# Kernel optimization log

Measured on AMD Instinct MI355X. Metric: run time of the kernel, lower is better.

The kernel has to match this reference:

```python
import jax, jax.numpy as jnp
import numpy as np

N_GRID = 128
DX = 1.0 / N_GRID
INV_DX = float(N_GRID)
DT = 1e-4
P_VOL = (DX * 0.5) ** 2
P_RHO = 1.0
P_MASS = P_VOL * P_RHO
E_MOD, NU = 1000.0, 0.2
MU_0 = E_MOD / (2.0 * (1.0 + NU))
LAMBDA_0 = E_MOD * NU / ((1.0 + NU) * (1.0 - 2.0 * NU))
N_PART = 1_000_000


def setup_inputs() -> dict:
    key = jax.random.key(0)
    k1, k2, k3, k4, k5 = jax.random.split(key, 5)
    # particles strictly inside the domain so the 3x3 stencil stays in-grid
    x = 0.1 + 0.8 * jax.random.uniform(k1, (N_PART, 2), jnp.float32)
    v = 0.5 * jax.random.normal(k2, (N_PART, 2), jnp.float32)
    C = 0.1 * jax.random.normal(k3, (N_PART, 2, 2), jnp.float32)
    F = jnp.eye(2, dtype=jnp.float32)[None] + 0.01 * jax.random.normal(k4, (N_PART, 2, 2), jnp.float32)
    material = jax.random.randint(k5, (N_PART,), 0, 3, jnp.int32)
    Jp = jnp.ones((N_PART,), jnp.float32)
    return {"x": x, "v": v, "C": C, "F": F, "material": material, "Jp": Jp}


def mpm_step(x, v, C, F, material, Jp):
    # --- particle kinematics / constitutive model ---
    base = jnp.floor(x * INV_DX - 0.5).astype(jnp.int32)          # (N,2)
    fx = x * INV_DX - base.astype(x.dtype)                        # (N,2)
    w = jnp.stack([0.5 * (1.5 - fx) ** 2,
                   0.75 - (fx - 1.0) ** 2,
                   0.5 * (fx - 0.5) ** 2], axis=0)                # (3,N,2)

    F = F + DT * jnp.einsum('nij,njk->nik', C, F)
    m0 = material == 0
    m2 = material == 2
    h = jnp.where(material == 1, 0.3, jnp.exp(10.0 * (1.0 - Jp)))
    mu = jnp.where(m0, 0.0, MU_0 * h)
    lam = LAMBDA_0 * h

    U, sig, Vh = jnp.linalg.svd(F)                                # batched 2x2 SVD
    clamped = jnp.clip(sig, 1.0 - 2.5e-2, 1.0 + 4.5e-3)
    Jp = jnp.where(m2, Jp * jnp.prod(sig / clamped, axis=-1), Jp)
    sig = jnp.where(m2[:, None], clamped, sig)
    J = jnp.prod(sig, axis=-1)

    eye = jnp.eye(2, dtype=F.dtype)
    F_liquid = eye[None] * jnp.sqrt(J)[:, None, None]             # J**(1/n_dim), n_dim=2
    F_snow = jnp.einsum('nij,nj,njk->nik', U, sig, Vh)
    F = jnp.where(m0[:, None, None], F_liquid,
                  jnp.where(m2[:, None, None], F_snow, F))

    R = jnp.einsum('nij,njk->nik', U, Vh)
    stress = (2.0 * mu[:, None, None] * jnp.einsum('nij,nkj->nik', F - R, F)
              + eye[None] * (lam * J * (J - 1.0))[:, None, None])
    stress = (-DT * P_VOL * 4.0 * INV_DX ** 2) * stress
    affine = stress + P_MASS * C                                  # (N,2,2)

    mom = P_MASS * v - jnp.einsum('nij,nj->ni', affine, x)        # (N,2)

    # --- P2G scatter over 3x3 stencil ---
    grid_v = jnp.zeros((N_GRID * N_GRID, 2), x.dtype)
    grid_m = jnp.zeros((N_GRID * N_GRID,), x.dtype)
    grid_aff = jnp.zeros((N_GRID * N_GRID, 2, 2), x.dtype)
    for i in range(3):
        for j in range(3):
            weight = w[i, :, 0] * w[j, :, 1]                      # (N,)
            idx = (base[:, 0] + i) * N_GRID + (base[:, 1] + j)
            grid_v = grid_v.at[idx].add(weight[:, None] * mom)
            grid_aff = grid_aff.at[idx].add(weight[:, None, None] * affine)
            grid_m = grid_m.at[idx].add(weight * P_MASS)
    grid_v = grid_v.reshape(N_GRID, N_GRID, 2)
    grid_m = grid_m.reshape(N_GRID, N_GRID)
    grid_aff = grid_aff.reshape(N_GRID, N_GRID, 2, 2)

    gi = jnp.arange(N_GRID, dtype=x.dtype)
    grid_x = jnp.stack(jnp.meshgrid(gi, gi, indexing='ij'), axis=-1) * DX   # (G,G,2)
    grid_v = grid_v + jnp.einsum('abij,abj->abi', grid_aff, grid_x)

    # --- grid normalization, gravity, boundary clamps ---
    nonempty = grid_m > 0
    safe_m = jnp.where(nonempty, grid_m, 1.0)
    grid_v = jnp.where(nonempty[..., None], grid_v / safe_m[..., None], grid_v)
    grid_v = grid_v.at[:, :, 1].add(jnp.where(nonempty, -DT * 50.0, 0.0))

    row = jnp.arange(N_GRID)
    vx, vy = grid_v[..., 0], grid_v[..., 1]
    vx = jnp.where(row[:, None] < 3, jnp.maximum(vx, 0.0), vx)
    vx = jnp.where(row[:, None] >= N_GRID - 2, jnp.minimum(vx, 0.0), vx)
    vy = jnp.where(row[None, :] < 3, jnp.maximum(vy, 0.0), vy)
    vy = jnp.where(row[None, :] >= N_GRID - 2, jnp.minimum(vy, 0.0), vy)
    grid_v = jnp.stack([vx, vy], axis=-1)

    # --- G2P gather over 3x3 stencil ---
    new_v = jnp.zeros_like(v)
    new_C = jnp.zeros_like(C)
    for i in range(3):
        for j in range(3):
            weight = w[i, :, 0] * w[j, :, 1]
            g_v = grid_v[base[:, 0] + i, base[:, 1] + j]          # (N,2)
            node = (base + jnp.array([i, j], base.dtype)).astype(x.dtype) * DX
            new_v = new_v + weight[:, None] * g_v
            new_C = new_C + weight[:, None, None] * g_v[:, :, None] * node[:, None, :]
    new_C = (new_C - new_v[:, :, None] * x[:, None, :]) * (4.0 * INV_DX ** 2)

    x_new = x + DT * new_v
    return x_new, new_v, new_C, F, material, Jp


def reference(x, v, C, F, material, Jp):
    return mpm_step(x, v, C, F, material, Jp)
```

## Files before the change

kernel.cpp:

```cpp
#include <hip/hip_runtime.h>

#define NPART 1000000
#define NGRID 128
#define NNODES (NGRID * NGRID)
#define NBINS 64
#define BINCAP 26624
#define SUBW 18
#define SUBN (SUBW * SUBW)
#define P2G_SUB 8
#define P2G_THREADS 512
#define PS_CHUNK 4
#define PS_BLOCKS 977

#define FPSCALE 281474976710656.0f
#define FPINV   3.552713678800501e-15

#define OUT_X   0
#define OUT_V   2000000
#define OUT_C   4000000
#define OUT_F   8000000
#define OUT_MAT 12000000
#define OUT_JP  13000000

__device__ __forceinline__ void quad_weights(float fx, float w[3]) {
    w[0] = 0.5f * (1.5f - fx) * (1.5f - fx);
    w[1] = 0.75f - (fx - 1.0f) * (fx - 1.0f);
    w[2] = 0.5f * (fx - 0.5f) * (fx - 0.5f);
}

struct PhysOut {
    float o00, o01, o10, o11;
    float aff00, aff01, aff10, aff11;
    float mom0, mom1;
    float jp_new;
};

__device__ __forceinline__ PhysOut particle_phys(
    float2 xx, float2 vv, float4 Cm, float4 Fin, int mat, float jp)
{
    const float DT = 1e-4f;
    const float P_MASS = 1.52587890625e-05f;
    const float MU_0 = (float)(1000.0 / (2.0 * 1.2));
    const float LAMBDA_0 = (float)(200.0 / 0.72);
    const float SCALE = -1e-4f;

    float F00 = Fin.x + DT * (Cm.x * Fin.x + Cm.y * Fin.z);
    float F01 = Fin.y + DT * (Cm.x * Fin.y + Cm.y * Fin.w);
    float F10 = Fin.z + DT * (Cm.z * Fin.x + Cm.w * Fin.z);
    float F11 = Fin.w + DT * (Cm.z * Fin.y + Cm.w * Fin.w);

    float h = (mat == 1) ? 0.3f : expf(10.0f * (1.0f - jp));
    float mu = (mat == 0) ? 0.0f : MU_0 * h;
    float lam = LAMBDA_0 * h;

    float Es = 0.5f * (F00 + F11), Fs = 0.5f * (F00 - F11);
    float Gs = 0.5f * (F01 + F10), Hs = 0.5f * (F10 - F01);
    float q2 = Es * Es + Hs * Hs;
    float r2 = Fs * Fs + Gs * Gs;
    float Qs = sqrtf(q2);
    float Rs = sqrtf(r2);
    float s1 = Qs + Rs, s2 = Qs - Rs;
    float cdif = 1.0f, sdif = 0.0f;
    if (q2 > 1e-30f) { float rq = 1.0f / Qs; cdif = Es * rq; sdif = Hs * rq; }
    float csum = 1.0f, ssum = 0.0f;
    if (r2 > 1e-30f) { float rr = 1.0f / Rs; csum = Fs * rr; ssum = Gs * rr; }
    float cucv = 0.5f * (cdif + csum);
    float susv = 0.5f * (cdif - csum);
    float cusv = 0.5f * (ssum - sdif);
    float sucv = 0.5f * (ssum + sdif);

    float c1 = fminf(fmaxf(s1, 1.0f - 2.5e-2f), 1.0f + 4.5e-3f);
    float c2 = fminf(fmaxf(s2, 1.0f - 2.5e-2f), 1.0f + 4.5e-3f);
    float jp_new = jp;
    float sg1 = s1, sg2 = s2;
    if (mat == 2) {
        jp_new = jp * (s1 / c1) * (s2 / c2);
        sg1 = c1;
        sg2 = c2;
    }
    float J = sg1 * sg2;

    float R00 = cdif, R01 = -sdif;
    float R10 = sdif, R11 = cdif;

    float o00, o01, o10, o11;
    if (mat == 0) {
        float sq = sqrtf(J);
        o00 = sq; o01 = 0.0f; o10 = 0.0f; o11 = sq;
    } else if (mat == 2) {
        o00 = sg1 * cucv + sg2 * susv;
        o01 = sg1 * cusv - sg2 * sucv;
        o10 = sg1 * sucv - sg2 * cusv;
        o11 = sg1 * susv + sg2 * cucv;
    } else {
        o00 = F00; o01 = F01; o10 = F10; o11 = F11;
    }

    float A00 = o00 - R00, A01 = o01 - R01, A10 = o10 - R10, A11 = o11 - R11;
    float S00 = A00 * o00 + A01 * o01;
    float S01 = A00 * o10 + A01 * o11;
    float S10 = A10 * o00 + A11 * o01;
    float S11 = A10 * o10 + A11 * o11;
    float ljj = lam * J * (J - 1.0f);

    PhysOut po;
    po.o00 = o00; po.o01 = o01; po.o10 = o10; po.o11 = o11;
    po.aff00 = SCALE * (2.0f * mu * S00 + ljj) + P_MASS * Cm.x;
    po.aff01 = SCALE * (2.0f * mu * S01)       + P_MASS * Cm.y;
    po.aff10 = SCALE * (2.0f * mu * S10)       + P_MASS * Cm.z;
    po.aff11 = SCALE * (2.0f * mu * S11 + ljj) + P_MASS * Cm.w;
    po.mom0 = P_MASS * vv.x - (po.aff00 * xx.x + po.aff01 * xx.y);
    po.mom1 = P_MASS * vv.y - (po.aff10 * xx.x + po.aff11 * xx.y);
    po.jp_new = jp_new;
    return po;
}

__device__ __forceinline__ int tile_of(float2 xx) {
    int b0 = (int)floorf(xx.x * 128.0f - 0.5f);
    int b1 = (int)floorf(xx.y * 128.0f - 0.5f);
    return ((b0 >> 4) << 3) | (b1 >> 4);
}

__global__ __launch_bounds__(256) void phys_scatter_kernel(
    const float2* __restrict__ x, const float2* __restrict__ v,
    const float4* __restrict__ C, const float4* __restrict__ F,
    const int* __restrict__ material, const float* __restrict__ Jp,
    int* __restrict__ binCursor, float* __restrict__ out, float4* __restrict__ rec)
{
    __shared__ int lh[NBINS];
    __shared__ int lbase[NBINS];
    int tid = threadIdx.x;
    if (tid < NBINS) lh[tid] = 0;
    __syncthreads();
    int base = blockIdx.x * (256 * PS_CHUNK);

    float2 xs[PS_CHUNK], vs[PS_CHUNK];
    float4 Cs[PS_CHUNK], Fs[PS_CHUNK];
    float jps[PS_CHUNK];
    int ms[PS_CHUNK], pk[PS_CHUNK];

    #pragma unroll
    for (int c = 0; c < PS_CHUNK; ++c) {
        int n = base + c * 256 + tid;
        if (n < NPART) {
            xs[c] = x[n]; vs[c] = v[n]; Cs[c] = C[n]; Fs[c] = F[n];
            ms[c] = material[n]; jps[c] = Jp[n];
            int t = tile_of(xs[c]);
            int r = atomicAdd(&lh[t], 1);
            pk[c] = (t << 16) | r;
        } else pk[c] = -1;
    }
    __syncthreads();
    if (tid < NBINS) {
        int c = lh[tid];
        lbase[tid] = c ? atomicAdd(&binCursor[tid], c) : 0;
    }
    __syncthreads();

    #pragma unroll
    for (int c = 0; c < PS_CHUNK; ++c) {
        if (pk[c] < 0) continue;
        int n = base + c * 256 + tid;
        PhysOut po = particle_phys(xs[c], vs[c], Cs[c], Fs[c], ms[c], jps[c]);
        ((float4*)(out + OUT_F))[n] = make_float4(po.o00, po.o01, po.o10, po.o11);
        out[OUT_MAT + n] = (float)ms[c];
        out[OUT_JP + n] = po.jp_new;
        int t = pk[c] >> 16, r = pk[c] & 0xffff;
        int pos = t * BINCAP + lbase[t] + r;
        rec[2 * pos]     = make_float4(xs[c].x, xs[c].y, po.mom0, po.mom1);
        rec[2 * pos + 1] = make_float4(po.aff00, po.aff01, po.aff10, po.aff11);
    }
}

__global__ __launch_bounds__(P2G_THREADS) void p2g_kernel(
    const float4* __restrict__ rec, const int* __restrict__ binCursor,
    float* __restrict__ gv, float* __restrict__ gm)
{
    __shared__ unsigned long long s_v0[SUBN], s_v1[SUBN], s_m[SUBN];
    int tid = threadIdx.x;
    int tile = blockIdx.x >> 3;
    int sub  = blockIdx.x & (P2G_SUB - 1);
    for (int i = tid; i < SUBN; i += P2G_THREADS) {
        s_v0[i] = 0ull; s_v1[i] = 0ull; s_m[i] = 0ull;
    }
    __syncthreads();
    int start = tile * BINCAP;
    int cnt = binCursor[tile];
    int t0 = (tile >> 3) << 4;
    int t1 = (tile & 7) << 4;
    const float DX = 1.0f / 128.0f;
    const float MASS_FP = 4294967296.0f;

    for (int p = sub * P2G_THREADS + tid; p < cnt; p += P2G_SUB * P2G_THREADS) {
        float4 r0 = rec[2 * (start + p)];
        float4 r1 = rec[2 * (start + p) + 1];
        float xg0 = r0.x * 128.0f, xg1 = r0.y * 128.0f;
        int b0 = (int)floorf(xg0 - 0.5f), b1 = (int)floorf(xg1 - 0.5f);
        float fx0 = xg0 - (float)b0, fx1 = xg1 - (float)b1;
        float wx[3], wy[3];
        quad_weights(fx0, wx);
        quad_weights(fx1, wy);
        int l0 = b0 - t0, l1 = b1 - t1;
        #pragma unroll
        for (int i = 0; i < 3; ++i) {
            float nx0 = (float)(b0 + i) * DX;
            #pragma unroll
            for (int j = 0; j < 3; ++j) {
                float wt = wx[i] * wy[j];
                float nx1 = (float)(b1 + j) * DX;
                int l = (l0 + i) * SUBW + (l1 + j);
                long long q0 = (long long)(wt * (r0.z + r1.x * nx0 + r1.y * nx1) * FPSCALE);
                long long q1 = (long long)(wt * (r0.w + r1.z * nx0 + r1.w * nx1) * FPSCALE);
                long long qm = (long long)(wt * MASS_FP);
                atomicAdd(&s_v0[l], (unsigned long long)q0);
                atomicAdd(&s_v1[l], (unsigned long long)q1);
                atomicAdd(&s_m[l], (unsigned long long)qm);
            }
        }
    }
    __syncthreads();
    for (int l = tid; l < SUBN; l += P2G_THREADS) {
        unsigned long long m = s_m[l];
        if (m != 0ull) {
            int gi = t0 + l / SUBW, gj = t1 + l % SUBW;
            if (gi < NGRID && gj < NGRID) {
                int g = gi * NGRID + gj;
                unsafeAtomicAdd(&gv[2 * g],     (float)((double)(long long)s_v0[l] * FPINV));
                unsafeAtomicAdd(&gv[2 * g + 1], (float)((double)(long long)s_v1[l] * FPINV));
                unsafeAtomicAdd(&gm[g],         (float)((double)(long long)m * FPINV));
            }
        }
    }
}

__global__ __launch_bounds__(256) void grid_kernel(
    float* __restrict__ gv, const float* __restrict__ gm)
{
    int idx = blockIdx.x * blockDim.x + threadIdx.x;
    if (idx >= NNODES) return;
    int i = idx >> 7, j = idx & 127;
    float m = gm[idx];
    float v0 = gv[2 * idx], v1 = gv[2 * idx + 1];
    if (m > 0.0f) {
        v0 /= m;
        v1 /= m;
        v1 -= 5e-3f;
    }
    if (i < 3) v0 = fmaxf(v0, 0.0f);
    if (i >= NGRID - 2) v0 = fminf(v0, 0.0f);
    if (j < 3) v1 = fmaxf(v1, 0.0f);
    if (j >= NGRID - 2) v1 = fminf(v1, 0.0f);
    gv[2 * idx] = v0;
    gv[2 * idx + 1] = v1;
}

__global__ __launch_bounds__(256) void g2p_kernel(
    const float2* __restrict__ x, const float* __restrict__ gv,
    float* __restrict__ out)
{
    int n = blockIdx.x * blockDim.x + threadIdx.x;
    if (n >= NPART) return;
    const float DX = 1.0f / 128.0f;
    const float DT = 1e-4f;
    const float K4 = 65536.0f;

    float2 xx = x[n];
    float xg0 = xx.x * 128.0f, xg1 = xx.y * 128.0f;
    int b0 = (int)floorf(xg0 - 0.5f), b1 = (int)floorf(xg1 - 0.5f);
    float fx0 = xg0 - (float)b0, fx1 = xg1 - (float)b1;
    float wx[3], wy[3];
    quad_weights(fx0, wx);
    quad_weights(fx1, wy);

    float nv0 = 0.f, nv1 = 0.f;
    float nC00 = 0.f, nC01 = 0.f, nC10 = 0.f, nC11 = 0.f;
    #pragma unroll
    for (int i = 0; i < 3; ++i) {
        float node0 = (float)(b0 + i) * DX;
        #pragma unroll
        for (int j = 0; j < 3; ++j) {
            float wt = wx[i] * wy[j];
            int idx = (b0 + i) * NGRID + (b1 + j);
            float g0 = gv[2 * idx], g1 = gv[2 * idx + 1];
            float node1 = (float)(b1 + j) * DX;
            nv0 += wt * g0;
            nv1 += wt * g1;
            nC00 += wt * g0 * node0;
            nC01 += wt * g0 * node1;
            nC10 += wt * g1 * node0;
            nC11 += wt * g1 * node1;
        }
    }
    nC00 = (nC00 - nv0 * xx.x) * K4;
    nC01 = (nC01 - nv0 * xx.y) * K4;
    nC10 = (nC10 - nv1 * xx.x) * K4;
    nC11 = (nC11 - nv1 * xx.y) * K4;

    ((float2*)(out + OUT_X))[n] = make_float2(xx.x + DT * nv0, xx.y + DT * nv1);
    ((float2*)(out + OUT_V))[n] = make_float2(nv0, nv1);
    ((float4*)(out + OUT_C))[n] = make_float4(nC00, nC01, nC10, nC11);
}

extern "C" void kernel_launch(void* const* d_in, const int* in_sizes, int n_in,
                              void* d_out, int out_size, void* d_ws, size_t ws_size,
                              hipStream_t stream)
{
    const float2* x = (const float2*)d_in[0];
    const float2* v = (const float2*)d_in[1];
    const float4* C = (const float4*)d_in[2];
    const float4* F = (const float4*)d_in[3];
    const int* material = (const int*)d_in[4];
    const float* Jp = (const float*)d_in[5];
    float* out = (float*)d_out;

    float* gv = (float*)d_ws;
    float* gm = gv + 2 * NNODES;
    int* binCursor = (int*)(gm + NNODES);
    float4* rec = (float4*)((char*)d_ws + (1 << 20));

    hipMemsetAsync(d_ws, 0, (size_t)(3 * NNODES) * sizeof(float) + NBINS * sizeof(int), stream);

    phys_scatter_kernel<<<PS_BLOCKS, 256, 0, stream>>>(x, v, C, F, material, Jp,
                                                       binCursor, out, rec);
    p2g_kernel<<<NBINS * P2G_SUB, P2G_THREADS, 0, stream>>>(rec, binCursor, gv, gm);
    grid_kernel<<<NNODES / 256, 256, 0, stream>>>(gv, gm);
    g2p_kernel<<<(NPART + 255) / 256, 256, 0, stream>>>(x, gv, out);
}
```

Measured before the change: 175.2 us.

## Replace global float atomics in P2G with per-block slabs reduced in grid kernel

Each P2G block now writes its full shared-memory subgrid to a private slab in global memory instead of issuing global float atomics. The grid kernel gathers and sums the up-to-4 overlapping tiles times 8 sub-blocks per node before normalising and applying the boundary conditions. Mass is accumulated as 32-bit integer weights in shared memory to cut shared-atomic width, and the memset of the grid buffers is dropped. This removes global atomic contention and most of the memset, at the cost of extra slab traffic and a heavier grid kernel.

```diff
diff --git a/kernel.cpp b/kernel.cpp
--- a/kernel.cpp
+++ b/kernel.cpp
@@ -14,6 +14,8 @@
 
 #define FPSCALE 281474976710656.0f
 #define FPINV   3.552713678800501e-15
+#define WSCALE  16777216.0f
+#define WINV    5.9604644775390625e-8
 
 #define OUT_X   0
 #define OUT_V   2000000
@@ -174,14 +176,15 @@
 
 __global__ __launch_bounds__(P2G_THREADS) void p2g_kernel(
     const float4* __restrict__ rec, const int* __restrict__ binCursor,
-    float* __restrict__ gv, float* __restrict__ gm)
-{
-    __shared__ unsigned long long s_v0[SUBN], s_v1[SUBN], s_m[SUBN];
+    float* __restrict__ part)
+{
+    __shared__ unsigned long long s_v0[SUBN], s_v1[SUBN];
+    __shared__ unsigned int s_m[SUBN];
     int tid = threadIdx.x;
     int tile = blockIdx.x >> 3;
     int sub  = blockIdx.x & (P2G_SUB - 1);
     for (int i = tid; i < SUBN; i += P2G_THREADS) {
-        s_v0[i] = 0ull; s_v1[i] = 0ull; s_m[i] = 0ull;
+        s_v0[i] = 0ull; s_v1[i] = 0ull; s_m[i] = 0u;
     }
     __syncthreads();
     int start = tile * BINCAP;
@@ -189,7 +192,6 @@
     int t0 = (tile >> 3) << 4;
     int t1 = (tile & 7) << 4;
     const float DX = 1.0f / 128.0f;
-    const float MASS_FP = 4294967296.0f;
 
     for (int p = sub * P2G_THREADS + tid; p < cnt; p += P2G_SUB * P2G_THREADS) {
         float4 r0 = rec[2 * (start + p)];
@@ -211,51 +213,67 @@
                 int l = (l0 + i) * SUBW + (l1 + j);
                 long long q0 = (long long)(wt * (r0.z + r1.x * nx0 + r1.y * nx1) * FPSCALE);
                 long long q1 = (long long)(wt * (r0.w + r1.z * nx0 + r1.w * nx1) * FPSCALE);
-                long long qm = (long long)(wt * MASS_FP);
+                unsigned int qm = (unsigned int)(wt * WSCALE);
                 atomicAdd(&s_v0[l], (unsigned long long)q0);
                 atomicAdd(&s_v1[l], (unsigned long long)q1);
-                atomicAdd(&s_m[l], (unsigned long long)qm);
+                atomicAdd(&s_m[l], qm);
             }
         }
     }
     __syncthreads();
+    float* slab = part + (size_t)blockIdx.x * (3 * SUBN);
     for (int l = tid; l < SUBN; l += P2G_THREADS) {
-        unsigned long long m = s_m[l];
-        if (m != 0ull) {
-            int gi = t0 + l / SUBW, gj = t1 + l % SUBW;
-            if (gi < NGRID && gj < NGRID) {
-                int g = gi * NGRID + gj;
-                unsafeAtomicAdd(&gv[2 * g],     (float)((double)(long long)s_v0[l] * FPINV));
-                unsafeAtomicAdd(&gv[2 * g + 1], (float)((double)(long long)s_v1[l] * FPINV));
-                unsafeAtomicAdd(&gm[g],         (float)((double)(long long)m * FPINV));
+        slab[l]            = (float)((double)(long long)s_v0[l] * FPINV);
+        slab[SUBN + l]     = (float)((double)(long long)s_v1[l] * FPINV);
+        slab[2 * SUBN + l] = (float)((double)s_m[l] * WINV);
+    }
+}
+
+__global__ __launch_bounds__(256) void grid_kernel(
+    const float* __restrict__ part, float2* __restrict__ gvn)
+{
+    int idx = blockIdx.x * blockDim.x + threadIdx.x;
+    if (idx >= NNODES) return;
+    const float P_MASS = 1.52587890625e-05f;
+    int gi = idx >> 7, gj = idx & 127;
+    int li = gi & 15, lj = gj & 15, ti = gi >> 4, tj = gj >> 4;
+
+    int tis[2], l0s[2]; int ni = 1; tis[0] = ti; l0s[0] = li;
+    if (li < 2 && ti > 0) { tis[1] = ti - 1; l0s[1] = li + 16; ni = 2; }
+    int tjs[2], l1s[2]; int nj = 1; tjs[0] = tj; l1s[0] = lj;
+    if (lj < 2 && tj > 0) { tjs[1] = tj - 1; l1s[1] = lj + 16; nj = 2; }
+
+    float s0 = 0.f, s1 = 0.f, sw = 0.f;
+    for (int a = 0; a < ni; ++a) {
+        for (int b = 0; b < nj; ++b) {
+            int tile2 = tis[a] * 8 + tjs[b];
+            int l = l0s[a] * SUBW + l1s[b];
+            const float* sb = part + (size_t)(tile2 * P2G_SUB) * (3 * SUBN) + l;
+            #pragma unroll
+            for (int sub = 0; sub < P2G_SUB; ++sub) {
+                s0 += sb[0];
+                s1 += sb[SUBN];
+                sw += sb[2 * SUBN];
+                sb += 3 * SUBN;
             }
         }
     }
-}
-
-__global__ __launch_bounds__(256) void grid_kernel(
-    float* __restrict__ gv, const float* __restrict__ gm)
-{
-    int idx = blockIdx.x * blockDim.x + threadIdx.x;
-    if (idx >= NNODES) return;
-    int i = idx >> 7, j = idx & 127;
-    float m = gm[idx];
-    float v0 = gv[2 * idx], v1 = gv[2 * idx + 1];
-    if (m > 0.0f) {
-        v0 /= m;
-        v1 /= m;
-        v1 -= 5e-3f;
-    }
-    if (i < 3) v0 = fmaxf(v0, 0.0f);
-    if (i >= NGRID - 2) v0 = fminf(v0, 0.0f);
-    if (j < 3) v1 = fmaxf(v1, 0.0f);
-    if (j >= NGRID - 2) v1 = fminf(v1, 0.0f);
-    gv[2 * idx] = v0;
-    gv[2 * idx + 1] = v1;
+    float m = sw * P_MASS;
+    if (m > 0.f) {
+        float rm = 1.0f / m;
+        s0 *= rm;
+        s1 *= rm;
+        s1 -= 5e-3f;
+    }
+    if (gi < 3) s0 = fmaxf(s0, 0.0f);
+    if (gi >= NGRID - 2) s0 = fminf(s0, 0.0f);
+    if (gj < 3) s1 = fmaxf(s1, 0.0f);
+    if (gj >= NGRID - 2) s1 = fminf(s1, 0.0f);
+    gvn[idx] = make_float2(s0, s1);
 }
 
 __global__ __launch_bounds__(256) void g2p_kernel(
-    const float2* __restrict__ x, const float* __restrict__ gv,
+    const float2* __restrict__ x, const float2* __restrict__ gvn,
     float* __restrict__ out)
 {
     int n = blockIdx.x * blockDim.x + threadIdx.x;
@@ -280,15 +298,14 @@
         #pragma unroll
         for (int j = 0; j < 3; ++j) {
             float wt = wx[i] * wy[j];
-            int idx = (b0 + i) * NGRID + (b1 + j);
-            float g0 = gv[2 * idx], g1 = gv[2 * idx + 1];
+            float2 g = gvn[(b0 + i) * NGRID + (b1 + j)];
             float node1 = (float)(b1 + j) * DX;
-            nv0 += wt * g0;
-            nv1 += wt * g1;
-            nC00 += wt * g0 * node0;
-            nC01 += wt * g0 * node1;
-            nC10 += wt * g1 * node0;
-            nC11 += wt * g1 * node1;
+            nv0 += wt * g.x;
+            nv1 += wt * g.y;
+            nC00 += wt * g.x * node0;
+            nC01 += wt * g.x * node1;
+            nC10 += wt * g.y * node0;
+            nC11 += wt * g.y * node1;
         }
     }
     nC00 = (nC00 - nv0 * xx.x) * K4;
@@ -313,16 +330,16 @@
     const float* Jp = (const float*)d_in[5];
     float* out = (float*)d_out;
 
-    float* gv = (float*)d_ws;
-    float* gm = gv + 2 * NNODES;
-    int* binCursor = (int*)(gm + NNODES);
-    float4* rec = (float4*)((char*)d_ws + (1 << 20));
-
-    hipMemsetAsync(d_ws, 0, (size_t)(3 * NNODES) * sizeof(float) + NBINS * sizeof(int), stream);
+    int* binCursor = (int*)d_ws;
+    float* part = (float*)((char*)d_ws + 4096);
+    float2* gvn = (float2*)((char*)d_ws + (11 << 18));
+    float4* rec = (float4*)((char*)d_ws + (4 << 20));
+
+    hipMemsetAsync(binCursor, 0, NBINS * sizeof(int), stream);
 
     phys_scatter_kernel<<<PS_BLOCKS, 256, 0, stream>>>(x, v, C, F, material, Jp,
                                                        binCursor, out, rec);
-    p2g_kernel<<<NBINS * P2G_SUB, P2G_THREADS, 0, stream>>>(rec, binCursor, gv, gm);
-    grid_kernel<<<NNODES / 256, 256, 0, stream>>>(gv, gm);
-    g2p_kernel<<<(NPART + 255) / 256, 256, 0, stream>>>(x, gv, out);
-}
+    p2g_kernel<<<NBINS * P2G_SUB, P2G_THREADS, 0, stream>>>(rec, binCursor, part);
+    grid_kernel<<<NNODES / 256, 256, 0, stream>>>(part, gvn);
+    g2p_kernel<<<(NPART + 255) / 256, 256, 0, stream>>>(x, gvn, out);
+}
```

Result: no change. 173.9 us (-0.7%).
